# Kernel optimization log

Hardware: AMD Instinct MI355X
Metric: run time of the kernel (lower is better)

Reference implementation:

```python
import jax, jax.numpy as jnp
import numpy as np

C = 1024
HEADS = 8
HEAD_DIM = C // HEADS
SCALE = HEAD_DIM ** -0.5
GROUPS = 32
EPS = 1e-5


def _conv3(x, w, b):
    # 3x3x3 conv, padding=1 (SAME), NCDHW
    y = jax.lax.conv_general_dilated(x, w, (1, 1, 1), 'SAME',
                                     dimension_numbers=('NCDHW', 'OIDHW', 'NCDHW'))
    return y + b[None, :, None, None, None]


def _proj(x, w, b):
    # 1x1x1 conv == channel matmul; w: (C_out, C_in)
    return jnp.einsum('oc,bcdhw->bodhw', w, x) + b[None, :, None, None, None]


def _gn(x, g, b):
    B, Ch, D, H, W = x.shape
    xr = x.reshape(B, GROUPS, Ch // GROUPS, D, H, W)
    mu = xr.mean(axis=(2, 3, 4, 5), keepdims=True)
    var = xr.var(axis=(2, 3, 4, 5), keepdims=True)
    xn = ((xr - mu) * jax.lax.rsqrt(var + EPS)).reshape(B, Ch, D, H, W)
    return xn * g[None, :, None, None, None] + b[None, :, None, None, None]


def _attn(q, k, v):
    # q,k,v: (B,C,D,H,W) -> heads over channels, tokens over flattened spatial
    B, Ch, D, H, W = q.shape
    S = D * H * W
    q = q.reshape(B, HEADS, HEAD_DIM, S)
    k = k.reshape(B, HEADS, HEAD_DIM, S)
    v = v.reshape(B, HEADS, HEAD_DIM, S)
    logits = jnp.einsum('bhds,bhdt->bhst', q, k) * SCALE  # (B,H,S,S)
    a = jax.nn.softmax(logits, axis=-1)
    o = jnp.einsum('bhst,bhdt->bhds', a, v)
    return o.reshape(B, Ch, D, H, W)


def setup_inputs() -> dict:
    key = jax.random.key(0)
    ks = iter(jax.random.split(key, 40))
    def w(shape, s=0.02):
        return jax.random.normal(next(ks), shape, dtype=jnp.float32) * s
    B, D, H, W = 2, 8, 16, 16
    inp = {'x': jax.random.normal(next(ks), (B, C, D, H, W), dtype=jnp.float32)}
    for side in ('l', 'r'):
        inp[f'conv_{side}_w'] = w((C, C, 3, 3, 3))
        inp[f'conv_{side}_b'] = jnp.zeros((C,), jnp.float32)
        inp[f'gn_{side}_g'] = jnp.ones((C,), jnp.float32)
        inp[f'gn_{side}_b'] = jnp.zeros((C,), jnp.float32)
    for name in ('ql', 'kr', 'vr', 'qr', 'kl', 'vl'):
        inp[f'{name}_w'] = w((C, C))
        inp[f'{name}_b'] = jnp.zeros((C,), jnp.float32)
    inp['fus_w'] = w((C, C))
    inp['fus_b'] = jnp.zeros((C,), jnp.float32)
    inp['gn_f_g'] = jnp.ones((C,), jnp.float32)
    inp['gn_f_b'] = jnp.zeros((C,), jnp.float32)
    return inp


def reference(x, conv_l_w, conv_l_b, gn_l_g, gn_l_b,
              conv_r_w, conv_r_b, gn_r_g, gn_r_b,
              ql_w, ql_b, kr_w, kr_b, vr_w, vr_b,
              qr_w, qr_b, kl_w, kl_b, vl_w, vl_b,
              fus_w, fus_b, gn_f_g, gn_f_b):
    W = x.shape[-1]
    mid = W // 2
    x_left = x[..., :mid]
    x_right = x[..., mid:2 * mid]
    f_l = jax.nn.relu(_gn(_conv3(x_left, conv_l_w, conv_l_b), gn_l_g, gn_l_b))
    f_r = jax.nn.relu(_gn(_conv3(x_right, conv_r_w, conv_r_b), gn_r_g, gn_r_b))
    rf = jnp.flip(f_r, axis=-1)
    # left attends to flipped right
    out_l = _attn(_proj(f_l, ql_w, ql_b), _proj(rf, kr_w, kr_b), _proj(rf, vr_w, vr_b))
    # flipped right attends to left
    out_r = _attn(_proj(rf, qr_w, qr_b), _proj(f_l, kl_w, kl_b), _proj(f_l, vl_w, vl_b))
    asym_map = jnp.abs(f_l - rf).mean(axis=1, keepdims=True)
    out_r = jnp.flip(out_r, axis=-1)
    f_concat = jnp.concatenate([out_l, out_r], axis=-1)  # W even -> no pad needed
    fused = jax.nn.relu(_gn(_proj(f_concat, fus_w, fus_b), gn_f_g, gn_f_b))
    return fused, asym_map
```

## Files before the change

kernel.cpp:

```cpp
#include <hip/hip_runtime.h>
#include <hip/hip_bf16.h>
#include <stdint.h>


using bf16_t = __bf16;
using bf16x4 = __attribute__((ext_vector_type(4))) __bf16;
using bf16x8 = __attribute__((ext_vector_type(8))) __bf16;
using f32x4  = __attribute__((ext_vector_type(4))) float;

typedef const uint32_t __attribute__((address_space(1)))* gas1_t;
typedef uint32_t __attribute__((address_space(3)))* las3_t;

__device__ __forceinline__ f32x4 mfma16(bf16x8 a, bf16x8 b, f32x4 c) {
  return __builtin_amdgcn_mfma_f32_16x16x32_bf16(a, b, c, 0, 0, 0);
}
__device__ __forceinline__ void gload_lds16(const void* g, void* l) {
  __builtin_amdgcn_global_load_lds((gas1_t)g, (las3_t)l, 16, 0, 0);
}

__global__ __launch_bounds__(256) void convw_kernel(
    const float* __restrict__ wl, const float* __restrict__ wr,
    bf16_t* __restrict__ Wb)
{
  const int chunk = blockIdx.x;
  const int co    = blockIdx.y;
  const int side  = blockIdx.z;
  const float* __restrict__ src = (side ? wr : wl) + (size_t)co * 27648 + (size_t)chunk * 6912;
  __shared__ float L[6912];
  __shared__ bf16_t Lb[27][260];
  const int tid = threadIdx.x;
  for (int i = tid; i < 1728; i += 256)
    *(float4*)&L[i << 2] = *(const float4*)&src[i << 2];
  __syncthreads();
  {
    const int ci = tid;
#pragma unroll
    for (int t = 0; t < 27; ++t)
      Lb[t][ci] = (bf16_t)L[ci * 27 + t];
  }
  __syncthreads();
  bf16_t* __restrict__ dst = Wb + (size_t)side * (1024u * 27648u) + (size_t)co * 27648 + (chunk << 8);
  for (int u = tid; u < 864; u += 256) {
    const int t = u >> 5, c8 = (u & 31) << 3;
    const bf16x8 v = *(const bf16x8*)&Lb[t][c8];
    *(bf16x8*)&dst[(t << 10) + c8] = v;
  }
}

__global__ __launch_bounds__(256) void projw_kernel(
    const float* ql, const float* kl, const float* kr, const float* qr,
    const float* vl, const float* vr, const float* fu,
    bf16_t* __restrict__ Wp, float qs)
{
  const int z = blockIdx.y;
  const float* src; float s = 1.f;
  switch (z) {
    case 0: src = ql; s = qs; break;
    case 1: src = kl; break;
    case 2: src = kr; break;
    case 3: src = qr; s = qs; break;
    case 4: src = vl; break;
    case 5: src = vr; break;
    default: src = fu; break;
  }
  const size_t i4 = ((size_t)blockIdx.x * 256 + threadIdx.x) * 4;
  const float4 v = *(const float4*)(src + i4);
  bf16x4 o;
  o[0] = (bf16_t)(v.x * s); o[1] = (bf16_t)(v.y * s);
  o[2] = (bf16_t)(v.z * s); o[3] = (bf16_t)(v.w * s);
  *(bf16x4*)(Wp + (size_t)z * 1048576 + i4) = o;
}

__global__ __launch_bounds__(256) void xp_build_kernel(
    const float* __restrict__ x, bf16_t* __restrict__ Xp)
{
  const int cc0  = blockIdx.x << 6;
  const int d    = blockIdx.y;
  const int sb   = blockIdx.z;
  const int side = sb >> 1, b = sb & 1;
  __shared__ bf16_t Tls[64][132];
  const int tid = threadIdx.x;
#pragma unroll
  for (int j = 0; j < 8; ++j) {
    const int u = tid + (j << 8);
    const int ci = u >> 5, sub = u & 31;
    const int hh = sub >> 1, half = sub & 1;
    const float4 v = *(const float4*)&x[((size_t)((b << 10) + cc0 + ci) * 8 + d) * 256 +
                                        (hh << 4) + (side << 3) + (half << 2)];
    bf16x4 o;
    o[0] = (bf16_t)v.x; o[1] = (bf16_t)v.y; o[2] = (bf16_t)v.z; o[3] = (bf16_t)v.w;
    *(bf16x4*)&Tls[ci][(hh << 3) + (half << 2)] = o;
  }
  __syncthreads();
  bf16_t* __restrict__ dst = Xp + (size_t)side * 3686400 + (size_t)b * 1843200;
#pragma unroll
  for (int j = 0; j < 4; ++j) {
    const int u = tid + (j << 8);
    const int hw = u >> 3, c8 = u & 7;
    const int hh = hw >> 3, ww = hw & 7;
    bf16x8 v;
#pragma unroll
    for (int e = 0; e < 8; ++e) v[e] = Tls[(c8 << 3) + e][hw];
    *(bf16x8*)&dst[(size_t)(((d + 1) * 18 + (hh + 1)) * 10 + (ww + 1)) * 1024 + cc0 + (c8 << 3)] = v;
  }
}

#define STAGE_A(BUF, H, TILE)                                                 \
  { const int koff_ = t0k + (TILE) * 64;                                      \
    gload_lds16(A + (size_t)arow[H][0] * 27648 + koff_ + swz,                 \
                &Al[BUF][((H) * 128 + (wv << 4)) << 6]);                      \
    gload_lds16(A + (size_t)arow[H][1] * 27648 + koff_ + swz,                 \
                &Al[BUF][(((H) * 128 + (wv << 4)) + 8) << 6]); }

#define STAGE_B(BUF, H, TILE)                                                 \
  { const int t_ = t0 + ((TILE) >> 4);                                        \
    const int tofs_ = ((t_ / 9) * 18 + ((t_ / 3) % 3)) * 10 + (t_ % 3);       \
    const int cb64_ = ((TILE) & 15) << 6;                                     \
    gload_lds16(X + (size_t)(browbase[H][0] + tofs_) * 1024 + cb64_ + swz,    \
                &Bl[BUF][((H) * 128 + (wv << 4)) << 6]);                      \
    gload_lds16(X + (size_t)(browbase[H][1] + tofs_) * 1024 + cb64_ + swz,    \
                &Bl[BUF][(((H) * 128 + (wv << 4)) + 8) << 6]); }

#define PHASE(BUF, MBASE, KS, RDB, VM, ...)                                   \
  { bf16x8 af[4];                                                             \
    _Pragma("unroll")                                                         \
    for (int m_ = 0; m_ < 4; ++m_) {                                          \
      const int row_ = (wm << 7) + (((MBASE) + m_) << 4) + lane15;            \
      const int ch_ = (((KS) << 2) + lane4) ^ (row_ & 7);                     \
      af[m_] = *(const bf16x8*)&Al[BUF][(row_ << 6) + (ch_ << 3)];            \
    }                                                                         \
    if (RDB) {                                                                \
      _Pragma("unroll")                                                       \
      for (int n_ = 0; n_ < 4; ++n_) {                                        \
        const int row_ = (wn << 6) + (n_ << 4) + lane15;                      \
        const int ch_ = (((KS) << 2) + lane4) ^ (row_ & 7);                   \
        bfr[n_] = *(const bf16x8*)&Bl[BUF][(row_ << 6) + (ch_ << 3)];         \
      }                                                                       \
    }                                                                         \
    __VA_ARGS__;                                                              \
    __builtin_amdgcn_s_barrier();                                             \
    asm volatile("s_waitcnt lgkmcnt(0)" ::: "memory");                        \
    __builtin_amdgcn_s_setprio(1);                                            \
    _Pragma("unroll")                                                         \
    for (int m_ = 0; m_ < 4; ++m_)                                            \
      _Pragma("unroll")                                                       \
      for (int n_ = 0; n_ < 4; ++n_)                                          \
        acc[(MBASE) + m_][n_] = mfma16(af[m_], bfr[n_], acc[(MBASE) + m_][n_]);\
    __builtin_amdgcn_s_setprio(0);                                            \
    if (VM) asm volatile("s_waitcnt vmcnt(2)" ::: "memory");                  \
    __builtin_amdgcn_s_barrier(); }

__global__ __launch_bounds__(512, 2) void conv8_kernel(
    const bf16_t* __restrict__ Wb, const bf16_t* __restrict__ Xp,
    bf16_t* __restrict__ Pb)
{
  const int bid = blockIdx.x;
  const int orig = (bid & 7) * 32 + (bid >> 3);
  const int ntile = orig & 7;
  const int mtile = (orig >> 3) & 3;
  const int side  = (orig >> 5) & 1;
  const int slice = orig >> 6;
  const int t0 = slice * 7;
  const int t0k = t0 << 10;
  const int NTT = (slice == 3) ? 96 : 112;
  const int n0 = ntile << 8;
  const int m0 = mtile << 8;
  const int b = n0 >> 10;

  const bf16_t* __restrict__ A = Wb + (size_t)side * 28311552u;
  const bf16_t* __restrict__ X = Xp + (size_t)side * 3686400 + (size_t)b * 1843200;

  __shared__ bf16_t Al[2][256 * 64];
  __shared__ bf16_t Bl[2][256 * 64];

  const int tid = threadIdx.x;
  const int lane = tid & 63;
  const int wv = tid >> 6;
  const int wm = wv >> 2, wn = wv & 3;
  const int lane15 = lane & 15, lane4 = lane >> 4;
  const int l8 = lane >> 3, l7 = lane & 7;
  const int swz = (l7 ^ l8) << 3;

  int arow[2][2], browbase[2][2];
#pragma unroll
  for (int h = 0; h < 2; ++h)
#pragma unroll
    for (int j = 0; j < 2; ++j) {
      const int r = h * 128 + (wv << 4) + (j << 3) + l8;
      arow[h][j] = m0 + r;
      const int c = n0 + r;
      const int d = (c >> 7) & 7, hh = (c >> 3) & 15, ww = c & 7;
      browbase[h][j] = (d * 18 + hh) * 10 + ww;
    }

  const f32x4 fz = {0.f, 0.f, 0.f, 0.f};
  f32x4 acc[8][4];
#pragma unroll
  for (int i = 0; i < 8; ++i)
#pragma unroll
    for (int j = 0; j < 4; ++j) acc[i][j] = fz;
  bf16x8 bfr[4];

  STAGE_B(0, 0, 0)
  STAGE_B(0, 1, 0)
  STAGE_A(0, 0, 0)
  STAGE_A(0, 1, 0)
  STAGE_B(1, 0, 1)
  asm volatile("s_waitcnt vmcnt(2)" ::: "memory");
  __builtin_amdgcn_s_barrier();

  const int NI = NTT >> 1;
  for (int i = 0; i < NI; ++i) {
    const int tB = 2 * i + 1;
    const int tn0 = 2 * i + 2, tn1 = 2 * i + 3;
    const bool pf = (i + 1 < NI);
    PHASE(0, 0, 0, true,  false, STAGE_B(1, 1, tB))
    PHASE(0, 4, 0, false, false, STAGE_A(1, 0, tB))
    PHASE(0, 0, 1, true,  false, STAGE_A(1, 1, tB))
    PHASE(0, 4, 1, false, true,  if (pf) STAGE_B(0, 0, tn0))
    PHASE(1, 0, 0, true,  false, if (pf) STAGE_B(0, 1, tn0))
    PHASE(1, 4, 0, false, false, if (pf) STAGE_A(0, 0, tn0))
    PHASE(1, 0, 1, true,  false, if (pf) STAGE_A(0, 1, tn0))
    PHASE(1, 4, 1, false, true,  if (pf) STAGE_B(1, 0, tn1))
  }

  bf16_t* __restrict__ P = Pb + (((size_t)(slice << 1) + side) << 21);
#pragma unroll
  for (int m = 0; m < 8; ++m) {
    const int row0 = m0 + (wm << 7) + (m << 4) + (lane4 << 2);
#pragma unroll
    for (int r = 0; r < 4; ++r) {
#pragma unroll
      for (int n = 0; n < 4; ++n) {
        const int col = n0 + (wn << 6) + (n << 4) + lane15;
        P[((size_t)(row0 + r) << 11) + col] = (bf16_t)acc[m][n][r];
      }
    }
  }
}

__global__ __launch_bounds__(256) void reduce4_kernel(
    const bf16_t* __restrict__ Pb, const float* __restrict__ bias_l,
    const float* __restrict__ bias_r, bf16_t* __restrict__ out_l, bf16_t* __restrict__ out_r,
    float* __restrict__ pS_lr, float* __restrict__ pQ_lr)
{
  const int id = blockIdx.x * 256 + threadIdx.x;
  const int tid = threadIdx.x;
  const int c8 = id & 255;
  const int co = (id >> 8) & 1023;
  const int side = id >> 18;
  const size_t off = ((size_t)co << 11) + ((size_t)c8 << 3);
  const float bia = (side ? bias_r : bias_l)[co];
  float acc[8];
#pragma unroll
  for (int e = 0; e < 8; ++e) acc[e] = bia;
#pragma unroll
  for (int s = 0; s < 4; ++s) {
    const bf16x8 v = *(const bf16x8*)&Pb[(((size_t)(s << 1) + side) << 21) + off];
#pragma unroll
    for (int e = 0; e < 8; ++e) acc[e] += (float)v[e];
  }
  bf16x8 ov;
#pragma unroll
  for (int e = 0; e < 8; ++e) ov[e] = (bf16_t)acc[e];
  *(bf16x8*)((side ? out_r : out_l) + off) = ov;
  float s = 0.f, q = 0.f;
#pragma unroll
  for (int e = 0; e < 8; ++e) { s += acc[e]; q += acc[e] * acc[e]; }
  __shared__ float sb[8];
  const int lane = tid & 63, wv = tid >> 6;
#pragma unroll
  for (int o = 1; o < 64; o <<= 1) { s += __shfl_xor(s, o, 64); q += __shfl_xor(q, o, 64); }
  if (lane == 0) { sb[wv] = s; sb[4 + wv] = q; }
  __syncthreads();
  if (tid == 0) {
    const int g = (side << 6) + (co >> 5);
    atomicAdd(&pS_lr[g],      sb[0] + sb[1]);
    atomicAdd(&pS_lr[g + 32], sb[2] + sb[3]);
    atomicAdd(&pQ_lr[g],      sb[4] + sb[5]);
    atomicAdd(&pQ_lr[g + 32], sb[6] + sb[7]);
  }
}

__device__ __forceinline__ void gemm_accum(
    const bf16_t* __restrict__ A, int lda,
    const bf16_t* __restrict__ Bt, int ldb,
    int K, f32x4 acc[4][4])
{
  __shared__ bf16_t Asm[128 * 64];
  __shared__ bf16_t Bsm[128 * 64];
  const int tid = threadIdx.x;
  const int lane = tid & 63;
  const int wv = tid >> 6;
  const int wm = wv >> 1, wn = wv & 1;
  const int lane15 = lane & 15, lane4 = lane >> 4;
  const int srow0 = (wv << 5) + (lane >> 3);
  const int sc = lane & 7;

  for (int k0 = 0; k0 < K; k0 += 64) {
#pragma unroll
    for (int i = 0; i < 4; ++i) {
      const int row = srow0 + (i << 3);
      gload_lds16(A + (size_t)row * lda + k0 + ((sc ^ (row & 7)) << 3),
                  &Asm[((wv << 2) + i) << 9]);
    }
#pragma unroll
    for (int i = 0; i < 4; ++i) {
      const int row = srow0 + (i << 3);
      gload_lds16(Bt + (size_t)row * ldb + k0 + ((sc ^ (row & 7)) << 3),
                  &Bsm[((wv << 2) + i) << 9]);
    }
    __syncthreads();
#pragma unroll
    for (int ks = 0; ks < 2; ++ks) {
      bf16x8 af[4];
#pragma unroll
      for (int mi = 0; mi < 4; ++mi) {
        const int row = (wm << 6) + (mi << 4) + lane15;
        const int ch = ((ks << 2) + lane4) ^ (row & 7);
        af[mi] = *(const bf16x8*)&Asm[(row << 6) + (ch << 3)];
      }
#pragma unroll
      for (int ni = 0; ni < 4; ++ni) {
        const int row = (wn << 6) + (ni << 4) + lane15;
        const int ch = ((ks << 2) + lane4) ^ (row & 7);
        const bf16x8 bfr = *(const bf16x8*)&Bsm[(row << 6) + (ch << 3)];
#pragma unroll
        for (int mi = 0; mi < 4; ++mi)
          acc[mi][ni] = mfma16(af[mi], bfr, acc[mi][ni]);
      }
    }
    __syncthreads();
  }
}

struct ProjTArgs {
  const bf16_t* act[2];
  const float*  bias[2][2];
  float         scl[2][2];
  bf16_t*       outp[2][2];
};
__global__ __launch_bounds__(256) void proj_t_kernel(const bf16_t* __restrict__ Wp, ProjTArgs a)
{
  const int side = blockIdx.z;
  const int n0 = blockIdx.x << 7;
  const int m0 = blockIdx.y << 7;
  const int seg = m0 >> 10;
  const f32x4 fz = {0.f, 0.f, 0.f, 0.f};
  f32x4 acc[4][4];
#pragma unroll
  for (int i = 0; i < 4; ++i)
#pragma unroll
    for (int j = 0; j < 4; ++j) acc[i][j] = fz;
  gemm_accum(a.act[side] + (size_t)n0 * 1024, 1024,
             Wp + (size_t)side * 2097152 + (size_t)m0 * 1024, 1024, 1024, acc);

  const int lane = threadIdx.x & 63, wv = threadIdx.x >> 6;
  const int wm = wv >> 1, wn = wv & 1;
  const int lane15 = lane & 15, lane4 = lane >> 4;
  const float* __restrict__ bias = a.bias[side][seg];
  const float bscale = a.scl[side][seg];
  bf16_t* __restrict__ C = a.outp[side][seg];
  const int mloc = (m0 & 1023) + (wn << 6);
  float bv[4];
#pragma unroll
  for (int ni = 0; ni < 4; ++ni) bv[ni] = bias[mloc + (ni << 4) + lane15] * bscale;
#pragma unroll
  for (int mi = 0; mi < 4; ++mi) {
    const int rowb = n0 + (wm << 6) + (mi << 4) + (lane4 << 2);
#pragma unroll
    for (int r = 0; r < 4; ++r) {
#pragma unroll
      for (int ni = 0; ni < 4; ++ni) {
        const int col = mloc + (ni << 4) + lane15;
        C[(size_t)(rowb + r) * 1024 + col] = (bf16_t)(acc[mi][ni][r] + bv[ni]);
      }
    }
  }
}

__global__ __launch_bounds__(256) void proj_v_kernel(
    const bf16_t* __restrict__ Wp, const bf16_t* __restrict__ flT,
    const bf16_t* __restrict__ rfT, const float* __restrict__ vlb,
    const float* __restrict__ vrb, bf16_t* __restrict__ Vl, bf16_t* __restrict__ Vr)
{
  const int side = blockIdx.z;
  const int m0 = blockIdx.x << 7;
  const int n0 = blockIdx.y << 7;
  const f32x4 fz = {0.f, 0.f, 0.f, 0.f};
  f32x4 acc[4][4];
#pragma unroll
  for (int i = 0; i < 4; ++i)
#pragma unroll
    for (int j = 0; j < 4; ++j) acc[i][j] = fz;
  gemm_accum(Wp + 4194304ull + (size_t)side * 1048576 + (size_t)m0 * 1024, 1024,
             (side ? rfT : flT) + (size_t)n0 * 1024, 1024, 1024, acc);

  const int lane = threadIdx.x & 63, wv = threadIdx.x >> 6;
  const int wm = wv >> 1, wn = wv & 1;
  const int lane15 = lane & 15, lane4 = lane >> 4;
  const float* __restrict__ bias = side ? vrb : vlb;
  bf16_t* __restrict__ C = side ? Vr : Vl;
#pragma unroll
  for (int mi = 0; mi < 4; ++mi) {
    const int row0 = m0 + (wm << 6) + (mi << 4) + (lane4 << 2);
#pragma unroll
    for (int r = 0; r < 4; ++r) {
      const float bia = bias[row0 + r];
#pragma unroll
      for (int ni = 0; ni < 4; ++ni) {
        const int col = n0 + (wn << 6) + (ni << 4) + lane15;
        C[(size_t)(row0 + r) * 2048 + col] = (bf16_t)(acc[mi][ni][r] + bia);
      }
    }
  }
}

__global__ __launch_bounds__(256) void fused_gemm_kernel(
    const bf16_t* __restrict__ Wf, const bf16_t* __restrict__ Bt, bf16_t* __restrict__ Pf)
{
  const int z = blockIdx.z;
  const int m0 = blockIdx.x << 7;
  const int n0 = blockIdx.y << 7;
  const f32x4 fz = {0.f, 0.f, 0.f, 0.f};
  f32x4 acc[4][4];
#pragma unroll
  for (int i = 0; i < 4; ++i)
#pragma unroll
    for (int j = 0; j < 4; ++j) acc[i][j] = fz;
  gemm_accum(Wf + (size_t)m0 * 1024 + (z << 9), 1024,
             Bt + (size_t)n0 * 1024 + (z << 9), 1024, 512, acc);

  const int lane = threadIdx.x & 63, wv = threadIdx.x >> 6;
  const int wm = wv >> 1, wn = wv & 1;
  const int lane15 = lane & 15, lane4 = lane >> 4;
  bf16_t* __restrict__ C = Pf + ((size_t)z << 22);
#pragma unroll
  for (int mi = 0; mi < 4; ++mi) {
    const int row0 = m0 + (wm << 6) + (mi << 4) + (lane4 << 2);
#pragma unroll
    for (int r = 0; r < 4; ++r) {
#pragma unroll
      for (int ni = 0; ni < 4; ++ni) {
        const int col = n0 + (wn << 6) + (ni << 4) + lane15;
        C[(size_t)(row0 + r) * 4096 + col] = (bf16_t)acc[mi][ni][r];
      }
    }
  }
}

__global__ __launch_bounds__(256) void gn_apply_lr_kernel(
    const bf16_t* __restrict__ yl, const bf16_t* __restrict__ yr,
    const float* __restrict__ gl, const float* __restrict__ bl,
    const float* __restrict__ gr, const float* __restrict__ br,
    const float* __restrict__ pS_lr, const float* __restrict__ pQ_lr,
    bf16_t* __restrict__ flT, bf16_t* __restrict__ rfT)
{
  const int side = blockIdx.z;
  const int n0 = blockIdx.x << 6;
  const int c0 = blockIdx.y << 6;
  const bf16_t* __restrict__ y = side ? yr : yl;
  const float* __restrict__ gamma = side ? gr : gl;
  const float* __restrict__ beta  = side ? br : bl;
  __shared__ float L[64][65];
  const int tid = threadIdx.x;
#pragma unroll
  for (int j = 0; j < 2; ++j) {
    const int u = tid + (j << 8);
    const int cr = u >> 3, ch = u & 7;
    const bf16x8 v = *(const bf16x8*)&y[(size_t)(c0 + cr) * 2048 + n0 + (ch << 3)];
#pragma unroll
    for (int e = 0; e < 8; ++e) L[cr][(ch << 3) + e] = (float)v[e];
  }
  __syncthreads();
  const int b = n0 >> 10;
  bf16_t* __restrict__ outT = side ? rfT : flT;
#pragma unroll
  for (int j = 0; j < 2; ++j) {
    const int u = tid + (j << 8);
    const int nr = u >> 3, c8 = u & 7;
    const int n = n0 + nr;
    const int nf = side ? ((n & ~7) | (7 - (n & 7))) : n;
    const int cbase = c0 + (c8 << 3);
    const int gidx = (side << 6) + (b << 5) + (cbase >> 5);
    const float m = pS_lr[gidx] * (1.f / 32768.f);
    const float rs = rsqrtf(pQ_lr[gidx] * (1.f / 32768.f) - m * m + 1e-5f);
    bf16x8 v;
#pragma unroll
    for (int e = 0; e < 8; ++e) {
      const int c = cbase + e;
      const float xv = (L[(c8 << 3) + e][nr] - m) * rs * gamma[c] + beta[c];
      v[e] = (bf16_t)fmaxf(xv, 0.f);
    }
    *(bf16x8*)&outT[(size_t)nf * 1024 + cbase] = v;
  }
}

__global__ __launch_bounds__(256, 2) void attn_kernel(
    const bf16_t* __restrict__ qlt, const bf16_t* __restrict__ krt, const bf16_t* __restrict__ vrm,
    const bf16_t* __restrict__ qrt, const bf16_t* __restrict__ klt, const bf16_t* __restrict__ vlm,
    bf16_t* __restrict__ xfc)
{
  const int st = blockIdx.x;
  const int bh = blockIdx.y;
  const int az = blockIdx.z;
  const int b = bh >> 3, h = bh & 7;
  const bf16_t* __restrict__ qt = az ? qrt : qlt;
  const bf16_t* __restrict__ kt = az ? klt : krt;
  const bf16_t* __restrict__ vm = az ? vlm : vrm;

  __shared__ bf16_t Ks[64 * 128];
  __shared__ bf16_t Vs[128 * 64];
  __shared__ bf16_t Ps[4][16 * 64];

  const int tid = threadIdx.x, lane = tid & 63, wv = tid >> 6;
  const int lane15 = lane & 15, lane4 = lane >> 4;

  bf16x8 qf[4];
  {
    const bf16_t* __restrict__ qbase = qt + (size_t)((b << 10) + (st << 6)) * 1024 + (h << 7);
    const int row = (wv << 4) + lane15;
#pragma unroll
    for (int kk = 0; kk < 4; ++kk)
      qf[kk] = *(const bf16x8*)&qbase[(size_t)row * 1024 + (kk << 5) + (lane4 << 3)];
  }

  const f32x4 fz = {0.f, 0.f, 0.f, 0.f};
  f32x4 oacc[8];
#pragma unroll
  for (int nj = 0; nj < 8; ++nj) oacc[nj] = fz;
  float mrun[4], lrun[4];
#pragma unroll
  for (int r = 0; r < 4; ++r) { mrun[r] = -3.0e38f; lrun[r] = 0.f; }

  for (int it = 0; it < 16; ++it) {
    __syncthreads();
#pragma unroll
    for (int j = 0; j < 4; ++j) {
      const int g = (wv << 2) + j;
      const int row = (g << 2) + lane4;
      gload_lds16(kt + (size_t)((b << 10) + (it << 6) + row) * 1024 + (h << 7) + ((lane15 ^ (row & 7)) << 3),
                  &Ks[g << 9]);
    }
#pragma unroll
    for (int j = 0; j < 4; ++j) {
      const int g = (wv << 2) + j;
      const int row = (g << 3) + (lane >> 3);
      gload_lds16(vm + (size_t)((h << 7) + row) * 2048 + (b << 10) + (it << 6) + (((lane & 7) ^ (row & 7)) << 3),
                  &Vs[g << 9]);
    }
    __syncthreads();
    f32x4 la[4];
#pragma unroll
    for (int tj = 0; tj < 4; ++tj) la[tj] = fz;
#pragma unroll
    for (int kk = 0; kk < 4; ++kk) {
#pragma unroll
      for (int tj = 0; tj < 4; ++tj) {
        const int row = (tj << 4) + lane15;
        const int ch = ((kk << 2) + lane4) ^ (row & 7);
        const bf16x8 kf = *(const bf16x8*)&Ks[(row << 7) + (ch << 3)];
        la[tj] = mfma16(qf[kk], kf, la[tj]);
      }
    }
    float mx[4];
    int ok = 1;
#pragma unroll
    for (int r = 0; r < 4; ++r) {
      float m_ = la[0][r];
#pragma unroll
      for (int tj = 1; tj < 4; ++tj) m_ = fmaxf(m_, la[tj][r]);
#pragma unroll
      for (int o = 1; o < 16; o <<= 1) m_ = fmaxf(m_, __shfl_xor(m_, o, 64));
      mx[r] = m_;
      ok &= (m_ <= mrun[r] + 8.f) ? 1 : 0;
    }
    if (!__all(ok)) {
#pragma unroll
      for (int r = 0; r < 4; ++r) {
        const float mnew = fmaxf(mrun[r], mx[r]);
        const float alpha = __builtin_amdgcn_exp2f(mrun[r] - mnew);
        mrun[r] = mnew;
        lrun[r] *= alpha;
#pragma unroll
        for (int nj = 0; nj < 8; ++nj) oacc[nj][r] *= alpha;
      }
    }
#pragma unroll
    for (int r = 0; r < 4; ++r) {
      const int row = (lane4 << 2) + r;
      float rs = 0.f;
#pragma unroll
      for (int tj = 0; tj < 4; ++tj) {
        const float p = __builtin_amdgcn_exp2f(la[tj][r] - mrun[r]);
        rs += p;
        const int byte_ = ((tj << 5) + (lane15 << 1)) ^ ((row & 7) << 4);
        *(bf16_t*)((char*)(&Ps[wv][0]) + (row << 7) + byte_) = (bf16_t)p;
      }
#pragma unroll
      for (int o = 1; o < 16; o <<= 1) rs += __shfl_xor(rs, o, 64);
      lrun[r] += rs;
    }
#pragma unroll
    for (int kk = 0; kk < 2; ++kk) {
      const int prow = lane15;
      const int pch = ((kk << 2) + lane4) ^ (prow & 7);
      const bf16x8 pf = *(const bf16x8*)&Ps[wv][(prow << 6) + (pch << 3)];
#pragma unroll
      for (int nj = 0; nj < 8; ++nj) {
        const int row = (nj << 4) + lane15;
        const int ch = ((kk << 2) + lane4) ^ (row & 7);
        const bf16x8 vf = *(const bf16x8*)&Vs[(row << 6) + (ch << 3)];
        oacc[nj] = mfma16(pf, vf, oacc[nj]);
      }
    }
  }
#pragma unroll
  for (int r = 0; r < 4; ++r) {
    const int sl = (wv << 4) + (lane4 << 2) + r;
    const int s = (st << 6) + sl;
    const int dd = s >> 7, hh2 = (s >> 3) & 15, ww = s & 7;
    const int w16 = az ? (15 - ww) : ww;
    const int n16 = (b << 11) + ((dd << 4) + hh2) * 16 + w16;
    const float inv = 1.f / lrun[r];
#pragma unroll
    for (int nj = 0; nj < 8; ++nj) {
      const int c = (h << 7) + (nj << 4) + lane15;
      xfc[(size_t)n16 * 1024 + c] = (bf16_t)(oacc[nj][r] * inv);
    }
  }
}

__global__ __launch_bounds__(256) void gn_partial_f_kernel(
    const bf16_t* __restrict__ Pf, const float* __restrict__ bias,
    float* __restrict__ pS, float* __restrict__ pQ)
{
  const int bg = blockIdx.x;
  const int sl = blockIdx.y;
  const int b = bg >> 5, g = bg & 31;
  const int tid = threadIdx.x;
  const int c = (g << 5) + (tid >> 3);
  const int s0 = (sl << 8) + ((tid & 7) << 5);
  const size_t base = (size_t)c * 4096 + (b << 11) + s0;
  const float bia = bias[c];
  float s = 0.f, q = 0.f;
#pragma unroll
  for (int u = 0; u < 4; ++u) {
    const bf16x8 v0 = *(const bf16x8*)&Pf[base + (u << 3)];
    const bf16x8 v1 = *(const bf16x8*)&Pf[base + (u << 3) + 4194304];
#pragma unroll
    for (int e = 0; e < 8; ++e) {
      const float v = (float)v0[e] + (float)v1[e] + bia;
      s += v; q += v * v;
    }
  }
  __shared__ float sb[8];
  const int lane = tid & 63, wv = tid >> 6;
#pragma unroll
  for (int o = 1; o < 64; o <<= 1) { s += __shfl_xor(s, o, 64); q += __shfl_xor(q, o, 64); }
  if (lane == 0) { sb[wv] = s; sb[4 + wv] = q; }
  __syncthreads();
  if (tid == 0) {
    pS[(bg << 3) + sl] = sb[0] + sb[1] + sb[2] + sb[3];
    pQ[(bg << 3) + sl] = sb[4] + sb[5] + sb[6] + sb[7];
  }
}

__global__ __launch_bounds__(256) void gn_apply_f_kernel(
    const bf16_t* __restrict__ Pf, const float* __restrict__ bias,
    const float* __restrict__ gamma, const float* __restrict__ beta,
    const float* __restrict__ pS, const float* __restrict__ pQ,
    float* __restrict__ outp)
{
  const int id = blockIdx.x * 256 + threadIdx.x;
  const int s8 = id & 255;
  const int c = (id >> 8) & 1023;
  const int b = id >> 18;
  const int gidx = (b << 5) + (c >> 5);
  float S = 0.f, Q = 0.f;
#pragma unroll
  for (int sl = 0; sl < 8; ++sl) { S += pS[(gidx << 3) + sl]; Q += pQ[(gidx << 3) + sl]; }
  const float m = S * (1.f / 65536.f);
  const float rs = rsqrtf(Q * (1.f / 65536.f) - m * m + 1e-5f);
  const float gm = gamma[c], bt = beta[c], bia = bias[c];
  const size_t idx = (size_t)c * 4096 + (b << 11) + (s8 << 3);
  const bf16x8 v0 = *(const bf16x8*)&Pf[idx];
  const bf16x8 v1 = *(const bf16x8*)&Pf[idx + 4194304];
  float o[8];
#pragma unroll
  for (int e = 0; e < 8; ++e) {
    const float v = (float)v0[e] + (float)v1[e] + bia;
    o[e] = fmaxf((v - m) * rs * gm + bt, 0.f);
  }
  float* __restrict__ op = &outp[(((size_t)(b << 10) + c) << 11) + (s8 << 3)];
  float4 o0, o1;
  o0.x = o[0]; o0.y = o[1]; o0.z = o[2]; o0.w = o[3];
  o1.x = o[4]; o1.y = o[5]; o1.z = o[6]; o1.w = o[7];
  *(float4*)op = o0;
  *(float4*)(op + 4) = o1;
}

__global__ __launch_bounds__(256) void asym_kernel(
    const bf16_t* __restrict__ flT, const bf16_t* __restrict__ rfT, float* __restrict__ outp)
{
  const int n = blockIdx.x;
  const int tid = threadIdx.x;
  const bf16x4 a = *(const bf16x4*)&flT[(size_t)n * 1024 + (tid << 2)];
  const bf16x4 c = *(const bf16x4*)&rfT[(size_t)n * 1024 + (tid << 2)];
  float s = 0.f;
#pragma unroll
  for (int e = 0; e < 4; ++e) s += fabsf((float)a[e] - (float)c[e]);
  __shared__ float sb[4];
  const int lane = tid & 63, wv = tid >> 6;
#pragma unroll
  for (int o = 1; o < 64; o <<= 1) s += __shfl_xor(s, o, 64);
  if (lane == 0) sb[wv] = s;
  __syncthreads();
  if (tid == 0) outp[n] = (sb[0] + sb[1] + sb[2] + sb[3]) * (1.f / 1024.f);
}

extern "C" void kernel_launch(void* const* d_in, const int* in_sizes, int n_in,
                              void* d_out, int out_size, void* d_ws, size_t ws_size,
                              hipStream_t stream)
{
  (void)in_sizes; (void)n_in; (void)out_size; (void)ws_size;
  const float* x    = (const float*)d_in[0];
  const float* clw  = (const float*)d_in[1];
  const float* clb  = (const float*)d_in[2];
  const float* glg  = (const float*)d_in[3];
  const float* glb_ = (const float*)d_in[4];
  const float* crw  = (const float*)d_in[5];
  const float* crb  = (const float*)d_in[6];
  const float* grg  = (const float*)d_in[7];
  const float* grb  = (const float*)d_in[8];
  const float* qlw = (const float*)d_in[9];  const float* qlb = (const float*)d_in[10];
  const float* krw = (const float*)d_in[11]; const float* krb = (const float*)d_in[12];
  const float* vrw = (const float*)d_in[13]; const float* vrb = (const float*)d_in[14];
  const float* qrw = (const float*)d_in[15]; const float* qrb = (const float*)d_in[16];
  const float* klw = (const float*)d_in[17]; const float* klb = (const float*)d_in[18];
  const float* vlw = (const float*)d_in[19]; const float* vlb = (const float*)d_in[20];
  const float* fuw = (const float*)d_in[21]; const float* fub = (const float*)d_in[22];
  const float* gfg = (const float*)d_in[23]; const float* gfb = (const float*)d_in[24];
  float* out = (float*)d_out;

  char* ws = (char*)d_ws;
  size_t off = 0;
  auto take = [&](size_t bytes) -> char* {
    char* p = ws + off; off += (bytes + 255) & ~(size_t)255; return p;
  };
  bf16_t* Wb    = (bf16_t*)take(113246208ull);
  bf16_t* Wp    = (bf16_t*)take(14680064ull);
  bf16_t* Xp    = (bf16_t*)take(14745600ull);
  float*  pS_lr = (float*) take(512);
  float*  pQ_lr = (float*) take(512);
  bf16_t* convL = (bf16_t*)take(4194304ull);
  bf16_t* convR = (bf16_t*)take(4194304ull);
  bf16_t* flT   = (bf16_t*)take(4194304ull);
  bf16_t* rfT   = (bf16_t*)take(4194304ull);
  float*  pS    = (float*) take(2048);
  float*  pQ    = (float*) take(2048);
  bf16_t* Pb    = (bf16_t*)take(33554432ull);

  char* al = (char*)Wb; size_t aoff = 0;
  auto takeA = [&](size_t bytes) -> char* {
    char* p = al + aoff; aoff += (bytes + 255) & ~(size_t)255; return p;
  };
  bf16_t* qlT = (bf16_t*)takeA(4194304ull);
  bf16_t* klT = (bf16_t*)takeA(4194304ull);
  bf16_t* krT = (bf16_t*)takeA(4194304ull);
  bf16_t* qrT = (bf16_t*)takeA(4194304ull);
  bf16_t* Vl  = (bf16_t*)takeA(4194304ull);
  bf16_t* Vr  = (bf16_t*)takeA(4194304ull);
  bf16_t* xfcT = (bf16_t*)takeA(8388608ull);
  bf16_t* Pf   = (bf16_t*)takeA(16777216ull);

  const float QS = 0.08838834764831843f * 1.4426950408889634f;

  hipMemsetAsync(Xp, 0, 14745600ull + 1024ull, stream);
  convw_kernel<<<dim3(4, 1024, 2), 256, 0, stream>>>(clw, crw, Wb);
  projw_kernel<<<dim3(1024, 7), 256, 0, stream>>>(qlw, klw, krw, qrw, vlw, vrw, fuw, Wp, QS);
  xp_build_kernel<<<dim3(16, 8, 4), 256, 0, stream>>>(x, Xp);
  conv8_kernel<<<dim3(256), 512, 0, stream>>>(Wb, Xp, Pb);
  reduce4_kernel<<<dim3(2048), 256, 0, stream>>>(Pb, clb, crb, convL, convR, pS_lr, pQ_lr);
  gn_apply_lr_kernel<<<dim3(32, 16, 2), 256, 0, stream>>>(convL, convR, glg, glb_, grg, grb,
                                                          pS_lr, pQ_lr, flT, rfT);
  ProjTArgs pa;
  pa.act[0] = flT; pa.act[1] = rfT;
  pa.bias[0][0] = qlb; pa.bias[0][1] = klb;
  pa.bias[1][0] = krb; pa.bias[1][1] = qrb;
  pa.scl[0][0] = QS;  pa.scl[0][1] = 1.f;
  pa.scl[1][0] = 1.f; pa.scl[1][1] = QS;
  pa.outp[0][0] = qlT; pa.outp[0][1] = klT;
  pa.outp[1][0] = krT; pa.outp[1][1] = qrT;
  proj_t_kernel<<<dim3(16, 16, 2), 256, 0, stream>>>(Wp, pa);
  proj_v_kernel<<<dim3(8, 16, 2), 256, 0, stream>>>(Wp, flT, rfT, vlb, vrb, Vl, Vr);

  attn_kernel<<<dim3(16, 16, 2), 256, 0, stream>>>(qlT, krT, Vr, qrT, klT, Vl, xfcT);
  fused_gemm_kernel<<<dim3(8, 32, 2), 256, 0, stream>>>(Wp + 6ull * 1048576, xfcT, Pf);
  gn_partial_f_kernel<<<dim3(64, 8), 256, 0, stream>>>(Pf, fub, pS, pQ);
  gn_apply_f_kernel<<<dim3(2048), 256, 0, stream>>>(Pf, fub, gfg, gfb, pS, pQ, out);
  asym_kernel<<<dim3(2048), 256, 0, stream>>>(flT, rfT, out + 4194304);
}
```

Before: 504.8 us.

## Deepen conv GEMM prefetch pipeline and batch LDS fragment reads per tile

Restructures the main loop of the conv GEMM kernel so that each LDS tile's A and B fragments for both k-halves are read up front. Later MFMA quarters then run without waiting on LDS. The global-to-LDS prefetch is also moved further ahead, with three stages issued before the loop and a vmcnt(6) wait instead of vmcnt(2), keeping more loads in flight. The last iteration is peeled out to drain the pipeline without conditional prefetches. This uses more VGPRs for the fragment buffers, which could cause spills under the 512-thread, 2-blocks-per-CU launch bound.

```diff
diff --git a/kernel.cpp b/kernel.cpp
--- a/kernel.cpp
+++ b/kernel.cpp
@@ -121,34 +121,39 @@
     gload_lds16(X + (size_t)(browbase[H][1] + tofs_) * 1024 + cb64_ + swz,    \
                 &Bl[BUF][(((H) * 128 + (wv << 4)) + 8) << 6]); }
 
-#define PHASE(BUF, MBASE, KS, RDB, VM, ...)                                   \
-  { bf16x8 af[4];                                                             \
+#define READ_B(BUF)                                                           \
+  _Pragma("unroll")                                                           \
+  for (int n_ = 0; n_ < 4; ++n_) {                                            \
+    const int row_ = (wn << 6) + (n_ << 4) + lane15;                          \
+    const int c0_ = lane4 ^ (row_ & 7);                                       \
+    const int c1_ = (4 + lane4) ^ (row_ & 7);                                 \
+    b0[n_] = *(const bf16x8*)&Bl[BUF][(row_ << 6) + (c0_ << 3)];              \
+    b1[n_] = *(const bf16x8*)&Bl[BUF][(row_ << 6) + (c1_ << 3)];              \
+  }
+
+#define READ_A(BUF, MBASE, D0, D1)                                           \
+  _Pragma("unroll")                                                           \
+  for (int m_ = 0; m_ < 4; ++m_) {                                            \
+    const int row_ = (wm << 7) + (((MBASE) + m_) << 4) + lane15;              \
+    const int c0_ = lane4 ^ (row_ & 7);                                       \
+    const int c1_ = (4 + lane4) ^ (row_ & 7);                                 \
+    D0[m_] = *(const bf16x8*)&Al[BUF][(row_ << 6) + (c0_ << 3)];              \
+    D1[m_] = *(const bf16x8*)&Al[BUF][(row_ << 6) + (c1_ << 3)];              \
+  }
+
+#define MFMAQ(MBASE, AR, BR)                                                  \
+  __builtin_amdgcn_s_setprio(1);                                              \
+  _Pragma("unroll")                                                           \
+  for (int m_ = 0; m_ < 4; ++m_)                                              \
     _Pragma("unroll")                                                         \
-    for (int m_ = 0; m_ < 4; ++m_) {                                          \
-      const int row_ = (wm << 7) + (((MBASE) + m_) << 4) + lane15;            \
-      const int ch_ = (((KS) << 2) + lane4) ^ (row_ & 7);                     \
-      af[m_] = *(const bf16x8*)&Al[BUF][(row_ << 6) + (ch_ << 3)];            \
-    }                                                                         \
-    if (RDB) {                                                                \
-      _Pragma("unroll")                                                       \
-      for (int n_ = 0; n_ < 4; ++n_) {                                        \
-        const int row_ = (wn << 6) + (n_ << 4) + lane15;                      \
-        const int ch_ = (((KS) << 2) + lane4) ^ (row_ & 7);                   \
-        bfr[n_] = *(const bf16x8*)&Bl[BUF][(row_ << 6) + (ch_ << 3)];         \
-      }                                                                       \
-    }                                                                         \
-    __VA_ARGS__;                                                              \
-    __builtin_amdgcn_s_barrier();                                             \
-    asm volatile("s_waitcnt lgkmcnt(0)" ::: "memory");                        \
-    __builtin_amdgcn_s_setprio(1);                                            \
-    _Pragma("unroll")                                                         \
-    for (int m_ = 0; m_ < 4; ++m_)                                            \
-      _Pragma("unroll")                                                       \
-      for (int n_ = 0; n_ < 4; ++n_)                                          \
-        acc[(MBASE) + m_][n_] = mfma16(af[m_], bfr[n_], acc[(MBASE) + m_][n_]);\
-    __builtin_amdgcn_s_setprio(0);                                            \
-    if (VM) asm volatile("s_waitcnt vmcnt(2)" ::: "memory");                  \
-    __builtin_amdgcn_s_barrier(); }
+    for (int n_ = 0; n_ < 4; ++n_)                                            \
+      acc[(MBASE) + m_][n_] = mfma16(AR[m_], BR[n_], acc[(MBASE) + m_][n_]);  \
+  __builtin_amdgcn_s_setprio(0);
+
+#define BAR __builtin_amdgcn_s_barrier()
+#define LGKM0 asm volatile("s_waitcnt lgkmcnt(0)" ::: "memory")
+#define VMC6 asm volatile("s_waitcnt vmcnt(6)" ::: "memory")
+#define VMC0 asm volatile("s_waitcnt vmcnt(0)" ::: "memory")
 
 __global__ __launch_bounds__(512, 2) void conv8_kernel(
     const bf16_t* __restrict__ Wb, const bf16_t* __restrict__ Xp,
@@ -199,29 +204,56 @@
   for (int i = 0; i < 8; ++i)
 #pragma unroll
     for (int j = 0; j < 4; ++j) acc[i][j] = fz;
-  bf16x8 bfr[4];
+  bf16x8 b0[4], b1[4], a0k0[4], a0k1[4], a4k0[4], a4k1[4];
 
   STAGE_B(0, 0, 0)
   STAGE_B(0, 1, 0)
   STAGE_A(0, 0, 0)
   STAGE_A(0, 1, 0)
   STAGE_B(1, 0, 1)
-  asm volatile("s_waitcnt vmcnt(2)" ::: "memory");
-  __builtin_amdgcn_s_barrier();
+  STAGE_B(1, 1, 1)
+  STAGE_A(1, 0, 1)
+  VMC6;
+  BAR;
 
   const int NI = NTT >> 1;
-  for (int i = 0; i < NI; ++i) {
-    const int tB = 2 * i + 1;
-    const int tn0 = 2 * i + 2, tn1 = 2 * i + 3;
-    const bool pf = (i + 1 < NI);
-    PHASE(0, 0, 0, true,  false, STAGE_B(1, 1, tB))
-    PHASE(0, 4, 0, false, false, STAGE_A(1, 0, tB))
-    PHASE(0, 0, 1, true,  false, STAGE_A(1, 1, tB))
-    PHASE(0, 4, 1, false, true,  if (pf) STAGE_B(0, 0, tn0))
-    PHASE(1, 0, 0, true,  false, if (pf) STAGE_B(0, 1, tn0))
-    PHASE(1, 4, 0, false, false, if (pf) STAGE_A(0, 0, tn0))
-    PHASE(1, 0, 1, true,  false, if (pf) STAGE_A(0, 1, tn0))
-    PHASE(1, 4, 1, false, true,  if (pf) STAGE_B(1, 0, tn1))
+  for (int i = 0; i < NI - 1; ++i) {
+    const int tA = 2 * i + 1, tN0 = 2 * i + 2, tN1 = 2 * i + 3;
+    READ_B(0) READ_A(0, 0, a0k0, a0k1)
+    STAGE_A(1, 1, tA)
+    BAR; LGKM0; MFMAQ(0, a0k0, b0) BAR;
+    READ_A(0, 4, a4k0, a4k1)
+    STAGE_B(0, 0, tN0)
+    BAR; LGKM0; MFMAQ(4, a4k0, b0) BAR;
+    STAGE_B(0, 1, tN0)
+    BAR; MFMAQ(0, a0k1, b1) BAR;
+    STAGE_A(0, 0, tN0)
+    BAR; MFMAQ(4, a4k1, b1) VMC6; BAR;
+    READ_B(1) READ_A(1, 0, a0k0, a0k1)
+    STAGE_A(0, 1, tN0)
+    BAR; LGKM0; MFMAQ(0, a0k0, b0) BAR;
+    READ_A(1, 4, a4k0, a4k1)
+    STAGE_B(1, 0, tN1)
+    BAR; LGKM0; MFMAQ(4, a4k0, b0) BAR;
+    STAGE_B(1, 1, tN1)
+    BAR; MFMAQ(0, a0k1, b1) BAR;
+    STAGE_A(1, 0, tN1)
+    BAR; MFMAQ(4, a4k1, b1) VMC6; BAR;
+  }
+  {
+    READ_B(0) READ_A(0, 0, a0k0, a0k1)
+    STAGE_A(1, 1, NTT - 1)
+    BAR; LGKM0; MFMAQ(0, a0k0, b0) BAR;
+    READ_A(0, 4, a4k0, a4k1)
+    BAR; LGKM0; MFMAQ(4, a4k0, b0) BAR;
+    BAR; MFMAQ(0, a0k1, b1) BAR;
+    BAR; MFMAQ(4, a4k1, b1) VMC0; BAR;
+    READ_B(1) READ_A(1, 0, a0k0, a0k1)
+    BAR; LGKM0; MFMAQ(0, a0k0, b0) BAR;
+    READ_A(1, 4, a4k0, a4k1)
+    BAR; LGKM0; MFMAQ(4, a4k0, b0) BAR;
+    BAR; MFMAQ(0, a0k1, b1) BAR;
+    BAR; MFMAQ(4, a4k1, b1) BAR;
   }
 
   bf16_t* __restrict__ P = Pb + (((size_t)(slice << 1) + side) << 21);
```

Measured after the change: 441.7 us. 12.5% less time.
